# Kernel optimization log

Measured on AMD Instinct MI355X. Metric: run time of the kernel, lower is better.

Reference implementation:

```python
import jax, jax.numpy as jnp
import numpy as np

# ---- static config (mirrors YOLOLayer init kwargs) ----
ANCHORS_ALL = jnp.array([[10.,13.],[16.,30.],[33.,23.],[30.,61.],[62.,45.],
                         [59.,119.],[116.,90.],[156.,198.],[373.,326.]], jnp.float32)
MASK = jnp.array([0, 1, 2], jnp.int32)
ANCHORS_PX = ANCHORS_ALL[:3]          # this scale's anchors, pixels
NUM_CLASSES = 1                       # forced by p_boxes.view(..., 6) in _first_loss
IMG_W = IMG_H = 608.0
B, A, GH, GW = 32, 3, 76, 76          # stride-8 head of a 608x608 YOLOv3
T = 48                                # number of ground-truth boxes
IGNORE_THRES = 0.5                    # ignore_thres_first_loss


def _bce(p, t):
    # torch BCELoss clamps log terms at -100
    return -(t * jnp.clip(jnp.log(p), -100.0) + (1.0 - t) * jnp.clip(jnp.log(1.0 - p), -100.0))


def _xywh2xyxy(b):
    xy, wh = b[..., :2], b[..., 2:4]
    return jnp.concatenate([xy - wh / 2, xy + wh / 2], -1)


def setup_inputs() -> dict:
    key = jax.random.key(0)
    k1, k2, k3 = jax.random.split(key, 3)
    x = jax.random.normal(k1, (B, A * (5 + NUM_CLASSES), GH, GW), jnp.float32) * 0.5
    # targets: [image_idx, cx, cy, w, h, cls], normalized coords; ids sorted, first = 0
    img_ids = jnp.sort(jnp.arange(T) % B).astype(jnp.float32)
    xy = jax.random.uniform(k2, (T, 2), minval=0.05, maxval=0.95)
    wh = jax.random.uniform(k3, (T, 2), minval=0.02, maxval=0.30)
    cls = jnp.zeros((T, 1), jnp.float32)
    target = jnp.concatenate([img_ids[:, None], xy, wh, cls], axis=1)
    return {"x": x, "target": target}


def _forward(x, target):
    stride_w, stride_h = IMG_W / GW, IMG_H / GH
    scale_anchors = ANCHORS_PX / jnp.array([stride_w, stride_h], jnp.float32)  # grid units

    pred = x.reshape(B, A, 5 + NUM_CLASSES, GH, GW).transpose(0, 1, 3, 4, 2)   # [B,A,H,W,5+C]
    cx = jax.nn.sigmoid(pred[..., 0]); cy = jax.nn.sigmoid(pred[..., 1])
    pw = pred[..., 2]; ph = pred[..., 3]
    pconf = jax.nn.sigmoid(pred[..., 4]); pcls = jax.nn.sigmoid(pred[..., 5:])

    # ---- __detect: decode boxes to pixel coords ----
    bx = cx + jnp.arange(GW, dtype=jnp.float32)[None, None, None, :]
    by = cy + jnp.arange(GH, dtype=jnp.float32)[None, None, :, None]
    bw = jnp.exp(pw) * scale_anchors[:, 0][None, :, None, None]
    bh = jnp.exp(ph) * scale_anchors[:, 1][None, :, None, None]
    boxes_px = jnp.stack([bx * stride_w, by * stride_h, bw * stride_w, bh * stride_h], -1).reshape(B, -1, 4)
    output = jnp.concatenate([boxes_px, pconf.reshape(B, -1, 1), pcls.reshape(B, -1, NUM_CLASSES)], -1)

    # ---- _first_loss: ignore mask from IoU(decoded preds, GT) in normalized coords ----
    timg = (target[:, 0] - target[0, 0]).astype(jnp.int32)                 # [T]
    tb = target[:, 1:5]                                                    # normalized xywh
    pbn = jnp.stack([bx / GW, by / GH, bw / GW, bh / GH], -1).reshape(B, -1, 4)  # [B,M,4]
    tc = _xywh2xyxy(tb)[:, None, None, :]                                  # [T,1,1,4]
    pc = _xywh2xyxy(pbn)[None]                                             # [1,B,M,4]
    iw = jnp.clip(jnp.minimum(tc[..., 2], pc[..., 2]) - jnp.maximum(tc[..., 0], pc[..., 0]), 0.0)
    ih = jnp.clip(jnp.minimum(tc[..., 3], pc[..., 3]) - jnp.maximum(tc[..., 1], pc[..., 1]), 0.0)
    inter = iw * ih
    ta = (tb[:, 2] * tb[:, 3])[:, None, None]
    pa = (pbn[..., 2] * pbn[..., 3])[None]
    iou = inter / (ta + pa - inter + 1e-16)                                # [T,B,M]
    match = timg[:, None] == jnp.arange(B)[None, :]                        # [T,B] GT-to-image
    best = jnp.max(jnp.where(match[:, :, None], iou, -1.0), 0)             # [B,M]
    ignore_mask = (best <= IGNORE_THRES).astype(jnp.float32).reshape(B, A, GH, GW)

    # ---- __build_target ----
    gxy = tb[:, :2] * jnp.array([GW, GH], jnp.float32)
    gwh = tb[:, 2:4] * jnp.array([GW, GH], jnp.float32)
    gwh_n = tb[:, 2:4]
    label = target[:, 5].astype(jnp.int32)
    an = ANCHORS_ALL / jnp.array([IMG_W, IMG_H], jnp.float32)              # [9,2] normalized
    w_inter = jnp.minimum(an[:, 0:1], gwh_n[None, :, 0]) * jnp.minimum(an[:, 1:2], gwh_n[None, :, 1])
    w_union = (an[:, 0] * an[:, 1] + 1e-16)[:, None] + (gwh_n[:, 0] * gwh_n[:, 1])[None, :] - w_inter
    anc_iou = w_inter / w_union                                            # [9,T]
    best_idx = jnp.argmax(anc_iou, 0)                                      # [T]
    gi = gxy[:, 0].astype(jnp.int32); gj = gxy[:, 1].astype(jnp.int32)
    in_mask = jnp.any(best_idx[:, None] == MASK[None, :], 1)
    valid = in_mask & (gi < GW) & (gj < GH) & (gi >= 0) & (gj >= 0)
    bi = best_idx - MASK[0]
    sc = 2.0 - gwh_n[:, 0] * gwh_n[:, 1]
    img_s = jnp.where(valid, timg, B)          # invalid rows -> OOB batch idx, dropped by scatter
    idx = (img_s, bi, gj, gi)

    z = jnp.zeros((B, A, GH, GW), jnp.float32)
    obj = z.at[idx].set(1.0, mode='drop')
    noobj = jnp.ones((B, A, GH, GW), jnp.float32).at[idx].set(0.0, mode='drop')
    tx = z.at[idx].set(gxy[:, 0] - jnp.floor(gxy[:, 0]), mode='drop')
    ty = z.at[idx].set(gxy[:, 1] - jnp.floor(gxy[:, 1]), mode='drop')
    tw = z.at[idx].set(jnp.log(gwh[:, 0] * stride_w / ANCHORS_PX[bi, 0] + 1e-16), mode='drop')
    th = z.at[idx].set(jnp.log(gwh[:, 1] * stride_h / ANCHORS_PX[bi, 1] + 1e-16), mode='drop')
    tconf = obj
    tcls = jnp.zeros((B, A, GH, GW, NUM_CLASSES), jnp.float32).at[img_s, bi, gj, gi, label].set(1.0, mode='drop')
    scale = jnp.ones((B, A, GH, GW), jnp.float32).at[idx].set(sc, mode='drop')

    # ignore_mask[obj==1] = 1 ; noobj_mask[ignore_mask==0] = 0
    ignore = jnp.where(obj > 0, 1.0, ignore_mask)
    noobj = jnp.where(ignore == 0, 0.0, noobj)

    s2 = scale * scale
    loss_x = jnp.sum(obj * (cx - tx) ** 2 * s2)
    loss_y = jnp.sum(obj * (cy - ty) ** 2 * s2)
    loss_w = jnp.sum(obj * (pw - tw) ** 2 * s2)
    loss_h = jnp.sum(obj * (ph - th) ** 2 * s2)
    loss_conf_obj = jnp.sum(obj * _bce(pconf, tconf))
    loss_conf_noobj = jnp.sum(noobj * _bce(pconf, tconf))
    loss_cls = jnp.sum(obj[..., None] * _bce(pcls, tcls))
    loss_conf = loss_conf_obj + loss_conf_noobj
    total = loss_x + loss_y + loss_w + loss_h + loss_conf + loss_cls
    r = lambda v: jnp.reshape(v, (1,))
    return (output, r(total), r(loss_x + loss_y), r(loss_w + loss_h), r(loss_conf), r(loss_cls))


def reference(x, target):
    return _forward(x, target)
```

## Files before the change

kernel.cpp:

```cpp
#include <hip/hip_runtime.h>

#define NB 32
#define NA 3
#define NGH 76
#define NGW 76
#define NT 48
#define PLANE (NGH * NGW)
#define NCELL (NB * NA * PLANE)
#define NOUT  (NCELL * 6)
#define CPT 4
#define BLK 192
#define NTHREAD (NCELL / CPT)
#define NBLKS (NTHREAD / BLK)
#define MAGIC 0x59A10C47u

static_assert(NTHREAD % BLK == 0, "grid must divide evenly");
static_assert(PLANE % CPT == 0, "4 consecutive cells stay in one plane row-chunk");
static_assert(4 * BLK >= NBLKS, "poll covers all flags in one unrolled pass");


__launch_bounds__(BLK)
__global__ void yolo_main(const float* __restrict__ x,
                          const float* __restrict__ tgt,
                          float* __restrict__ out,
                          float* __restrict__ partials,
                          unsigned int* __restrict__ flags,
                          float* __restrict__ lossbuf) {
    __shared__ float st[NT * 16];
    __shared__ unsigned long long sball[NB];
    __shared__ int soff[NB + 1];
    __shared__ int sord[NT];
    __shared__ float red[3][4];

    const int tx  = threadIdx.x;
    const int bid = blockIdx.x;
    const int tid = bid * BLK + tx;
    const int g   = tid * CPT;

    const int gw0 = g % NGW;
    const int gh  = (g / NGW) % NGH;
    const int a   = (g / PLANE) % NA;
    const int b   = g / (NA * PLANE);

    const float* xp = x + (size_t)(b * (NA * 6) + a * 6) * PLANE + (g % PLANE);
    const float4 v0 = *(const float4*)(xp);
    const float4 v1 = *(const float4*)(xp + PLANE);
    const float4 v2 = *(const float4*)(xp + 2 * PLANE);
    const float4 v3 = *(const float4*)(xp + 3 * PLANE);
    const float4 v4 = *(const float4*)(xp + 4 * PLANE);
    const float4 v5 = *(const float4*)(xp + 5 * PLANE);

    if (tx < 64) {
        const int t = tx;
        const bool isT = (t < NT);
        int timg = 999;
        if (isT) {
            const float t00 = tgt[0];
            const float* tr = tgt + t * 6;
            timg = (int)(tr[0] - t00);
            const float bxn = tr[1], byn = tr[2], bwn = tr[3], bhn = tr[4];

            const float gx = bxn * (float)NGW;
            const float gy = byn * (float)NGH;
            const int gi = (int)gx;
            const int gj = (int)gy;
            const float tarea = bwn * bhn;

            const float aw_px[9] = {10.f,16.f,33.f,30.f,62.f,59.f,116.f,156.f,373.f};
            const float ah_px[9] = {13.f,30.f,23.f,61.f,45.f,119.f,90.f,198.f,326.f};
            int bidx = 0; float biou = -1e30f;
            #pragma unroll
            for (int k = 0; k < 9; ++k) {
                const float aw = aw_px[k] / 608.0f;
                const float ah = ah_px[k] / 608.0f;
                const float wi = fminf(aw, bwn) * fminf(ah, bhn);
                const float un = ((aw * ah + 1e-16f) + tarea) - wi;
                const float iou = wi / un;
                if (iou > biou) { biou = iou; bidx = k; }
            }
            const bool inm = (bidx >= 0) && (bidx <= 2);
            const bool valid = inm && (gi < NGW) && (gj < NGH) && (gi >= 0) && (gj >= 0);
            const int bic = bidx < 0 ? 0 : (bidx > 2 ? 2 : bidx);
            const float apw = (bic == 0) ? 10.f : ((bic == 1) ? 16.f : 33.f);
            const float aph = (bic == 0) ? 13.f : ((bic == 1) ? 30.f : 23.f);

            float* s = st + t * 16;
            s[0]  = (float)timg;
            s[1]  = valid ? 1.0f : 0.0f;
            s[2]  = (float)bidx;
            s[3]  = (float)gj;
            s[4]  = (float)gi;
            s[5]  = gx - floorf(gx);
            s[6]  = gy - floorf(gy);
            s[7]  = __logf(((bwn * (float)NGW) * 8.0f) / apw + 1e-16f);
            s[8]  = __logf(((bhn * (float)NGH) * 8.0f) / aph + 1e-16f);
            s[9]  = 2.0f - bwn * bhn;
            s[10] = bxn - bwn * 0.5f;
            s[11] = byn - bhn * 0.5f;
            s[12] = bxn + bwn * 0.5f;
            s[13] = byn + bhn * 0.5f;
            s[14] = tarea;
            s[15] = 0.0f;
        }

        int cnt = 0;
        for (int bb = 0; bb < NB; ++bb) {
            const unsigned long long m = __ballot(timg == bb);
            if (t == 0) sball[bb] = m;
            if (t == bb) cnt = (int)__popcll(m);
        }
        int inc = cnt;
        #pragma unroll
        for (int d = 1; d < 32; d <<= 1) {
            const int v = __shfl_up(inc, d);
            if (t >= d) inc += v;
        }
        if (t < NB) soff[t] = inc - cnt;
        if (t == NB - 1) soff[NB] = inc;
        if (isT) {
            const unsigned long long m = sball[timg];
            const int rank = (int)__popcll(m & ((1ULL << t) - 1ULL));
            sord[soff[timg] + rank] = t;
        }
    }

    const float p0[CPT] = {v0.x, v0.y, v0.z, v0.w};
    const float p1[CPT] = {v1.x, v1.y, v1.z, v1.w};
    const float p2[CPT] = {v2.x, v2.y, v2.z, v2.w};
    const float p3[CPT] = {v3.x, v3.y, v3.z, v3.w};
    const float p4[CPT] = {v4.x, v4.y, v4.z, v4.w};
    const float p5[CPT] = {v5.x, v5.y, v5.z, v5.w};

    const float sa_w = (a == 0) ? 1.25f  : ((a == 1) ? 2.0f  : 4.125f);
    const float sa_h = (a == 0) ? 1.625f : ((a == 1) ? 3.75f : 2.875f);

    float cxv[CPT], cyv[CPT], pcf[CPT], pcl[CPT];
    float px1[CPT], py1[CPT], px2[CPT], py2[CPT], par[CPT];
    float o24[CPT * 6];

    #pragma unroll
    for (int c = 0; c < CPT; ++c) {
        const float cx    = 1.0f / (1.0f + __expf(-p0[c]));
        const float cy    = 1.0f / (1.0f + __expf(-p1[c]));
        const float pconf = 1.0f / (1.0f + __expf(-p4[c]));
        const float pcls  = 1.0f / (1.0f + __expf(-p5[c]));
        const float bx = cx + (float)(gw0 + c);
        const float by = cy + (float)gh;
        const float bw = __expf(p2[c]) * sa_w;
        const float bh = __expf(p3[c]) * sa_h;

        o24[c * 6 + 0] = bx * 8.0f;
        o24[c * 6 + 1] = by * 8.0f;
        o24[c * 6 + 2] = bw * 8.0f;
        o24[c * 6 + 3] = bh * 8.0f;
        o24[c * 6 + 4] = pconf;
        o24[c * 6 + 5] = pcls;

        const float pxc = bx * (1.0f / NGW), pyc = by * (1.0f / NGH);
        const float pwn = bw * (1.0f / NGW), phn = bh * (1.0f / NGH);
        cxv[c] = cx; cyv[c] = cy; pcf[c] = pconf; pcl[c] = pcls;
        px1[c] = pxc - pwn * 0.5f; py1[c] = pyc - phn * 0.5f;
        px2[c] = pxc + pwn * 0.5f; py2[c] = pyc + phn * 0.5f;
        par[c] = pwn * phn;
    }

    {
        float4* ob = (float4*)(out + (size_t)g * 6);
        #pragma unroll
        for (int k = 0; k < 6; ++k)
            ob[k] = make_float4(o24[4 * k], o24[4 * k + 1], o24[4 * k + 2], o24[4 * k + 3]);
    }

    __syncthreads();

    float best[CPT] = {-1.f, -1.f, -1.f, -1.f};
    int   so[CPT]   = {-1, -1, -1, -1};
    {
        const int j1 = soff[b + 1];
        for (int j = soff[b]; j < j1; ++j) {
            const int t = sord[j];
            const float* s = st + t * 16;
            const float s1 = s[1], s2f = s[2], s3f = s[3], s4f = s[4];
            const float x1 = s[10], y1 = s[11], x2 = s[12], y2 = s[13], ta = s[14];
            const bool vmatch = (s1 != 0.0f) && ((int)s2f == a) && ((int)s3f == gh);
            #pragma unroll
            for (int c = 0; c < CPT; ++c) {
                const float iw = fmaxf(fminf(x2, px2[c]) - fmaxf(x1, px1[c]), 0.0f);
                const float ih = fmaxf(fminf(y2, py2[c]) - fmaxf(y1, py1[c]), 0.0f);
                const float inter = iw * ih;
                const float iou = inter / (((ta + par[c]) - inter) + 1e-16f);
                if (iou > best[c]) best[c] = iou;
                if (vmatch && ((int)s4f == gw0 + c)) so[c] = t;
            }
        }
    }

    float lxy = 0.f, lwh = 0.f, lconf = 0.f, lcls = 0.f;
    #pragma unroll
    for (int c = 0; c < CPT; ++c) {
        if (so[c] >= 0) {
            const float* s = st + so[c] * 16;
            const float sc = s[9], s2 = sc * sc;
            const float dx = cxv[c] - s[5], dy = cyv[c] - s[6];
            const float dw = p2[c] - s[7], dh = p3[c] - s[8];
            lxy   += (dx * dx + dy * dy) * s2;
            lwh   += (dw * dw + dh * dh) * s2;
            lconf += -fmaxf(__logf(pcf[c]), -100.0f);
            lcls  += -fmaxf(__logf(pcl[c]), -100.0f);
        } else if (best[c] <= 0.5f) {
            lconf += -fmaxf(__logf(1.0f - pcf[c]), -100.0f);
        }
    }

    #pragma unroll
    for (int off = 32; off > 0; off >>= 1) {
        lxy   += __shfl_down(lxy, off);
        lwh   += __shfl_down(lwh, off);
        lconf += __shfl_down(lconf, off);
        lcls  += __shfl_down(lcls, off);
    }
    const int lane = tx & 63, wv = tx >> 6;
    if (lane == 0) { red[wv][0] = lxy; red[wv][1] = lwh; red[wv][2] = lconf; red[wv][3] = lcls; }
    __syncthreads();
    if (tx == 0) {
        __hip_atomic_store(&partials[bid * 4 + 0], red[0][0] + red[1][0] + red[2][0], __ATOMIC_RELAXED, __HIP_MEMORY_SCOPE_AGENT);
        __hip_atomic_store(&partials[bid * 4 + 1], red[0][1] + red[1][1] + red[2][1], __ATOMIC_RELAXED, __HIP_MEMORY_SCOPE_AGENT);
        __hip_atomic_store(&partials[bid * 4 + 2], red[0][2] + red[1][2] + red[2][2], __ATOMIC_RELAXED, __HIP_MEMORY_SCOPE_AGENT);
        __hip_atomic_store(&partials[bid * 4 + 3], red[0][3] + red[1][3] + red[2][3], __ATOMIC_RELAXED, __HIP_MEMORY_SCOPE_AGENT);
        asm volatile("s_waitcnt vmcnt(0)" ::: "memory");
        __hip_atomic_store(&flags[bid], MAGIC, __ATOMIC_RELAXED, __HIP_MEMORY_SCOPE_AGENT);
    }

    if (bid == 0) {
        for (;;) {
            const unsigned f0 = __hip_atomic_load(&flags[tx], __ATOMIC_RELAXED, __HIP_MEMORY_SCOPE_AGENT);
            const unsigned f1 = __hip_atomic_load(&flags[tx + BLK], __ATOMIC_RELAXED, __HIP_MEMORY_SCOPE_AGENT);
            const unsigned f2 = __hip_atomic_load(&flags[tx + 2 * BLK], __ATOMIC_RELAXED, __HIP_MEMORY_SCOPE_AGENT);
            const unsigned f3 = (tx + 3 * BLK < NBLKS)
                ? __hip_atomic_load(&flags[tx + 3 * BLK], __ATOMIC_RELAXED, __HIP_MEMORY_SCOPE_AGENT)
                : MAGIC;
            const int ok = (f0 == MAGIC) & (f1 == MAGIC) & (f2 == MAGIC) & (f3 == MAGIC);
            if (__syncthreads_and(ok)) break;
            __builtin_amdgcn_s_sleep(16);
        }

        float a0 = 0.f, a1 = 0.f, a2 = 0.f, a3 = 0.f;
        #pragma unroll
        for (int k = 0; k < 4; ++k) {
            const int i = tx + k * BLK;
            if (i < NBLKS) {
                const float q0 = __hip_atomic_load(&partials[i * 4 + 0], __ATOMIC_RELAXED, __HIP_MEMORY_SCOPE_AGENT);
                const float q1 = __hip_atomic_load(&partials[i * 4 + 1], __ATOMIC_RELAXED, __HIP_MEMORY_SCOPE_AGENT);
                const float q2 = __hip_atomic_load(&partials[i * 4 + 2], __ATOMIC_RELAXED, __HIP_MEMORY_SCOPE_AGENT);
                const float q3 = __hip_atomic_load(&partials[i * 4 + 3], __ATOMIC_RELAXED, __HIP_MEMORY_SCOPE_AGENT);
                a0 += q0; a1 += q1; a2 += q2; a3 += q3;
            }
        }
        #pragma unroll
        for (int off = 32; off > 0; off >>= 1) {
            a0 += __shfl_down(a0, off);
            a1 += __shfl_down(a1, off);
            a2 += __shfl_down(a2, off);
            a3 += __shfl_down(a3, off);
        }
        if (lane == 0) { red[wv][0] = a0; red[wv][1] = a1; red[wv][2] = a2; red[wv][3] = a3; }
        __syncthreads();
        if (tx == 0) {
            const float s0 = red[0][0] + red[1][0] + red[2][0];
            const float s1 = red[0][1] + red[1][1] + red[2][1];
            const float s2 = red[0][2] + red[1][2] + red[2][2];
            const float s3 = red[0][3] + red[1][3] + red[2][3];
            lossbuf[1] = s0;
            lossbuf[2] = s1;
            lossbuf[3] = s2;
            lossbuf[4] = s3;
            lossbuf[0] = ((s0 + s1) + s2) + s3;
        }
    }
}

extern "C" void kernel_launch(void* const* d_in, const int* in_sizes, int n_in,
                              void* d_out, int out_size, void* d_ws, size_t ws_size,
                              hipStream_t stream) {
    const float* x   = (const float*)d_in[0];
    const float* tgt = (const float*)d_in[1];
    float* out          = (float*)d_out;
    float* lossbuf      = out + NOUT;
    float* partials     = (float*)d_ws;
    unsigned int* flags = (unsigned int*)(partials + NBLKS * 4);

    hipLaunchKernelGGL(yolo_main, dim3(NBLKS), dim3(BLK), 0, stream,
                       x, tgt, out, partials, flags, lossbuf);
    (void)in_sizes; (void)n_in; (void)out_size; (void)ws_size;
}
```

Before: 16.41 us.

## Interleave cell-to-thread mapping so each wave reads contiguous per-channel scalars

Changes the cell assignment from four consecutive cells per thread, read as float4, to four cells strided by 64 within each wave's 256-cell tile. Input reads become per-lane scalar loads that coalesce across the wave, and output writes become an 8-byte-aligned 4-float store plus a 2-float store. Each slot now decodes its own batch, anchor and grid coordinates and runs its own target loop, so the target-list loop runs up to four times per thread instead of once. This trades wide vector loads for coalesced narrow ones and adds index arithmetic and repeated target-loop overhead.

```diff
diff --git a/kernel.cpp b/kernel.cpp
--- a/kernel.cpp
+++ b/kernel.cpp
@@ -8,15 +8,17 @@
 #define PLANE (NGH * NGW)
 #define NCELL (NB * NA * PLANE)
 #define NOUT  (NCELL * 6)
-#define CPT 4
+#define SLOT 4
 #define BLK 192
-#define NTHREAD (NCELL / CPT)
-#define NBLKS (NTHREAD / BLK)
+#define TILE (BLK * SLOT)
+#define NBLKS (NCELL / TILE)
 #define MAGIC 0x59A10C47u
 
-static_assert(NTHREAD % BLK == 0, "grid must divide evenly");
-static_assert(PLANE % CPT == 0, "4 consecutive cells stay in one plane row-chunk");
+static_assert(NCELL % TILE == 0, "grid must divide evenly");
 static_assert(4 * BLK >= NBLKS, "poll covers all flags in one unrolled pass");
+
+typedef float f4a8 __attribute__((vector_size(16), aligned(8)));
+typedef float f2v  __attribute__((vector_size(8)));
 
 
 __launch_bounds__(BLK)
@@ -34,21 +36,25 @@
 
     const int tx  = threadIdx.x;
     const int bid = blockIdx.x;
-    const int tid = bid * BLK + tx;
-    const int g   = tid * CPT;
-
-    const int gw0 = g % NGW;
-    const int gh  = (g / NGW) % NGH;
-    const int a   = (g / PLANE) % NA;
-    const int b   = g / (NA * PLANE);
-
-    const float* xp = x + (size_t)(b * (NA * 6) + a * 6) * PLANE + (g % PLANE);
-    const float4 v0 = *(const float4*)(xp);
-    const float4 v1 = *(const float4*)(xp + PLANE);
-    const float4 v2 = *(const float4*)(xp + 2 * PLANE);
-    const float4 v3 = *(const float4*)(xp + 3 * PLANE);
-    const float4 v4 = *(const float4*)(xp + 4 * PLANE);
-    const float4 v5 = *(const float4*)(xp + 5 * PLANE);
+    const int l   = tx & 63, w = tx >> 6;
+    const int cb  = bid * TILE + w * 256 + l;
+
+    int   cells[SLOT], bb4[SLOT], aa4[SLOT], gh4[SLOT], gw4[SLOT];
+    float p[SLOT][6];
+    #pragma unroll
+    for (int k = 0; k < SLOT; ++k) {
+        const int cell = cb + k * 64;
+        const int b_  = cell / (NA * PLANE);
+        const int r_  = cell - b_ * (NA * PLANE);
+        const int a_  = r_ / PLANE;
+        const int pc  = r_ - a_ * PLANE;
+        const int gh_ = pc / NGW;
+        const int gw_ = pc - gh_ * NGW;
+        cells[k] = cell; bb4[k] = b_; aa4[k] = a_; gh4[k] = gh_; gw4[k] = gw_;
+        const float* base = x + (size_t)(b_ * (NA * 6) + a_ * 6) * PLANE + pc;
+        #pragma unroll
+        for (int ch = 0; ch < 6; ++ch) p[k][ch] = base[ch * PLANE];
+    }
 
     if (tx < 64) {
         const int t = tx;
@@ -124,91 +130,68 @@
         }
     }
 
-    const float p0[CPT] = {v0.x, v0.y, v0.z, v0.w};
-    const float p1[CPT] = {v1.x, v1.y, v1.z, v1.w};
-    const float p2[CPT] = {v2.x, v2.y, v2.z, v2.w};
-    const float p3[CPT] = {v3.x, v3.y, v3.z, v3.w};
-    const float p4[CPT] = {v4.x, v4.y, v4.z, v4.w};
-    const float p5[CPT] = {v5.x, v5.y, v5.z, v5.w};
-
-    const float sa_w = (a == 0) ? 1.25f  : ((a == 1) ? 2.0f  : 4.125f);
-    const float sa_h = (a == 0) ? 1.625f : ((a == 1) ? 3.75f : 2.875f);
-
-    float cxv[CPT], cyv[CPT], pcf[CPT], pcl[CPT];
-    float px1[CPT], py1[CPT], px2[CPT], py2[CPT], par[CPT];
-    float o24[CPT * 6];
-
-    #pragma unroll
-    for (int c = 0; c < CPT; ++c) {
-        const float cx    = 1.0f / (1.0f + __expf(-p0[c]));
-        const float cy    = 1.0f / (1.0f + __expf(-p1[c]));
-        const float pconf = 1.0f / (1.0f + __expf(-p4[c]));
-        const float pcls  = 1.0f / (1.0f + __expf(-p5[c]));
-        const float bx = cx + (float)(gw0 + c);
-        const float by = cy + (float)gh;
-        const float bw = __expf(p2[c]) * sa_w;
-        const float bh = __expf(p3[c]) * sa_h;
-
-        o24[c * 6 + 0] = bx * 8.0f;
-        o24[c * 6 + 1] = by * 8.0f;
-        o24[c * 6 + 2] = bw * 8.0f;
-        o24[c * 6 + 3] = bh * 8.0f;
-        o24[c * 6 + 4] = pconf;
-        o24[c * 6 + 5] = pcls;
+    float cxv[SLOT], cyv[SLOT], pcf[SLOT], pcl[SLOT];
+    float px1[SLOT], py1[SLOT], px2[SLOT], py2[SLOT], par[SLOT];
+    #pragma unroll
+    for (int k = 0; k < SLOT; ++k) {
+        const int a_ = aa4[k];
+        const float sa_w = (a_ == 0) ? 1.25f  : ((a_ == 1) ? 2.0f  : 4.125f);
+        const float sa_h = (a_ == 0) ? 1.625f : ((a_ == 1) ? 3.75f : 2.875f);
+
+        const float cx    = 1.0f / (1.0f + __expf(-p[k][0]));
+        const float cy    = 1.0f / (1.0f + __expf(-p[k][1]));
+        const float pconf = 1.0f / (1.0f + __expf(-p[k][4]));
+        const float pcls  = 1.0f / (1.0f + __expf(-p[k][5]));
+        const float bx = cx + (float)gw4[k];
+        const float by = cy + (float)gh4[k];
+        const float bw = __expf(p[k][2]) * sa_w;
+        const float bh = __expf(p[k][3]) * sa_h;
+
+        float* op = out + (size_t)cells[k] * 6;
+        const f4a8 oa = {bx * 8.0f, by * 8.0f, bw * 8.0f, bh * 8.0f};
+        const f2v  ob = {pconf, pcls};
+        *(f4a8*)op       = oa;
+        *(f2v*)(op + 4)  = ob;
 
         const float pxc = bx * (1.0f / NGW), pyc = by * (1.0f / NGH);
         const float pwn = bw * (1.0f / NGW), phn = bh * (1.0f / NGH);
-        cxv[c] = cx; cyv[c] = cy; pcf[c] = pconf; pcl[c] = pcls;
-        px1[c] = pxc - pwn * 0.5f; py1[c] = pyc - phn * 0.5f;
-        px2[c] = pxc + pwn * 0.5f; py2[c] = pyc + phn * 0.5f;
-        par[c] = pwn * phn;
-    }
-
-    {
-        float4* ob = (float4*)(out + (size_t)g * 6);
-        #pragma unroll
-        for (int k = 0; k < 6; ++k)
-            ob[k] = make_float4(o24[4 * k], o24[4 * k + 1], o24[4 * k + 2], o24[4 * k + 3]);
+        cxv[k] = cx; cyv[k] = cy; pcf[k] = pconf; pcl[k] = pcls;
+        px1[k] = pxc - pwn * 0.5f; py1[k] = pyc - phn * 0.5f;
+        px2[k] = pxc + pwn * 0.5f; py2[k] = pyc + phn * 0.5f;
+        par[k] = pwn * phn;
     }
 
     __syncthreads();
 
-    float best[CPT] = {-1.f, -1.f, -1.f, -1.f};
-    int   so[CPT]   = {-1, -1, -1, -1};
-    {
-        const int j1 = soff[b + 1];
-        for (int j = soff[b]; j < j1; ++j) {
+    float lxy = 0.f, lwh = 0.f, lconf = 0.f, lcls = 0.f;
+    #pragma unroll
+    for (int k = 0; k < SLOT; ++k) {
+        float best = -1.0f;
+        int so = -1;
+        const int b_ = bb4[k];
+        const int j1 = soff[b_ + 1];
+        for (int j = soff[b_]; j < j1; ++j) {
             const int t = sord[j];
             const float* s = st + t * 16;
-            const float s1 = s[1], s2f = s[2], s3f = s[3], s4f = s[4];
-            const float x1 = s[10], y1 = s[11], x2 = s[12], y2 = s[13], ta = s[14];
-            const bool vmatch = (s1 != 0.0f) && ((int)s2f == a) && ((int)s3f == gh);
-            #pragma unroll
-            for (int c = 0; c < CPT; ++c) {
-                const float iw = fmaxf(fminf(x2, px2[c]) - fmaxf(x1, px1[c]), 0.0f);
-                const float ih = fmaxf(fminf(y2, py2[c]) - fmaxf(y1, py1[c]), 0.0f);
-                const float inter = iw * ih;
-                const float iou = inter / (((ta + par[c]) - inter) + 1e-16f);
-                if (iou > best[c]) best[c] = iou;
-                if (vmatch && ((int)s4f == gw0 + c)) so[c] = t;
-            }
-        }
-    }
-
-    float lxy = 0.f, lwh = 0.f, lconf = 0.f, lcls = 0.f;
-    #pragma unroll
-    for (int c = 0; c < CPT; ++c) {
-        if (so[c] >= 0) {
-            const float* s = st + so[c] * 16;
+            const float iw = fmaxf(fminf(s[12], px2[k]) - fmaxf(s[10], px1[k]), 0.0f);
+            const float ih = fmaxf(fminf(s[13], py2[k]) - fmaxf(s[11], py1[k]), 0.0f);
+            const float inter = iw * ih;
+            const float iou = inter / (((s[14] + par[k]) - inter) + 1e-16f);
+            if (iou > best) best = iou;
+            if (s[1] != 0.0f && (int)s[2] == aa4[k] && (int)s[3] == gh4[k] && (int)s[4] == gw4[k])
+                so = t;
+        }
+        if (so >= 0) {
+            const float* s = st + so * 16;
             const float sc = s[9], s2 = sc * sc;
-            const float dx = cxv[c] - s[5], dy = cyv[c] - s[6];
-            const float dw = p2[c] - s[7], dh = p3[c] - s[8];
+            const float dx = cxv[k] - s[5], dy = cyv[k] - s[6];
+            const float dw = p[k][2] - s[7], dh = p[k][3] - s[8];
             lxy   += (dx * dx + dy * dy) * s2;
             lwh   += (dw * dw + dh * dh) * s2;
-            lconf += -fmaxf(__logf(pcf[c]), -100.0f);
-            lcls  += -fmaxf(__logf(pcl[c]), -100.0f);
-        } else if (best[c] <= 0.5f) {
-            lconf += -fmaxf(__logf(1.0f - pcf[c]), -100.0f);
+            lconf += -fmaxf(__logf(pcf[k]), -100.0f);
+            lcls  += -fmaxf(__logf(pcl[k]), -100.0f);
+        } else if (best <= 0.5f) {
+            lconf += -fmaxf(__logf(1.0f - pcf[k]), -100.0f);
         }
     }
 
@@ -219,8 +202,7 @@
         lconf += __shfl_down(lconf, off);
         lcls  += __shfl_down(lcls, off);
     }
-    const int lane = tx & 63, wv = tx >> 6;
-    if (lane == 0) { red[wv][0] = lxy; red[wv][1] = lwh; red[wv][2] = lconf; red[wv][3] = lcls; }
+    if (l == 0) { red[w][0] = lxy; red[w][1] = lwh; red[w][2] = lconf; red[w][3] = lcls; }
     __syncthreads();
     if (tx == 0) {
         __hip_atomic_store(&partials[bid * 4 + 0], red[0][0] + red[1][0] + red[2][0], __ATOMIC_RELAXED, __HIP_MEMORY_SCOPE_AGENT);
@@ -263,7 +245,7 @@
             a2 += __shfl_down(a2, off);
             a3 += __shfl_down(a3, off);
         }
-        if (lane == 0) { red[wv][0] = a0; red[wv][1] = a1; red[wv][2] = a2; red[wv][3] = a3; }
+        if (l == 0) { red[w][0] = a0; red[w][1] = a1; red[w][2] = a2; red[w][3] = a3; }
         __syncthreads();
         if (tx == 0) {
             const float s0 = red[0][0] + red[1][0] + red[2][0];
```

New measurement: 16.89 us. 2.9% more time.
